# Kernel optimization log

Measured on AMD Instinct MI355X. Metric: run time of the kernel, lower is better.

## Reference

```python
import jax, jax.numpy as jnp
import numpy as np

B, H, W = 256, 512, 512
KH, KW = 16, 16
OH, OW = 8, 8
N = (H // KH) * (W // KW)  # 1024 chunks
KIN = KH * KW              # 256
KOUT = OH * OW             # 64


def setup_inputs() -> dict:
    key = jax.random.key(0)
    kx, kw, kb = jax.random.split(key, 3)
    x = jax.random.normal(kx, (B, H, W), dtype=jnp.float32)
    # Per-chunk Linear weights, torch-style uniform(-1/sqrt(fan_in), 1/sqrt(fan_in))
    bound = 1.0 / np.sqrt(KIN)
    Wk = jax.random.uniform(kw, (N, KOUT, KIN), dtype=jnp.float32, minval=-bound, maxval=bound)
    bk = jax.random.uniform(kb, (N, KOUT), dtype=jnp.float32, minval=-bound, maxval=bound)
    return {"x": x, "Wk": Wk, "bk": bk}


def _split_chunks(x):
    # [B,H,W] -> [B, N, KH, KW] matching split_matrix_in_chunks
    b = x.shape[0]
    return (x.reshape(b, H // KH, KH, W // KW, KW)
             .swapaxes(2, 3)
             .reshape(b, N, KH, KW))


def _recombine(chunks):
    # [B, N, OH, OW] -> [B, s*OH, s*OW] matching recombine_chunks_into_matrix
    b = chunks.shape[0]
    s = int(np.sqrt(N))
    return (chunks.reshape(b, s, s, OH, OW)
                  .swapaxes(3, 2)
                  .reshape(b, s * OH, s * OW))


def reference(x, Wk, bk):
    xc = _split_chunks(x).reshape(-1, N, KIN)          # [B,N,KIN]
    # grouped GEMM: one Linear per chunk, fused with bias + ReLU
    y = jnp.einsum('bnk,nok->bno', xc, Wk) + bk[None]  # [B,N,KOUT]
    y = jax.nn.relu(y)
    out = _recombine(y.reshape(-1, N, OH, OW))         # [B, s*OH, s*OW]
    b, h, w = out.shape
    return out.reshape(b, h * w)
```

## Files before the change

### kernel.cpp

```cpp
#include <hip/hip_runtime.h>


typedef __bf16 bf16x8 __attribute__((ext_vector_type(8)));
typedef float  f32x4  __attribute__((ext_vector_type(4)));

constexpr int LDW = 264;

union bfpack { unsigned short s[8]; bf16x8 v; };

__device__ __forceinline__ unsigned short f2bf(float f) {
  union { float f; unsigned u; } v; v.f = f;
  unsigned r = v.u + 0x7fffu + ((v.u >> 16) & 1u);
  return (unsigned short)(r >> 16);
}

typedef __attribute__((address_space(1))) const void GV;
typedef __attribute__((address_space(3))) void LV;

__global__ __launch_bounds__(256, 2) void comp_kernel(
    const float* __restrict__ x, const float* __restrict__ Wk,
    const float* __restrict__ bk, float* __restrict__ out) {
  __shared__ unsigned short Ws[64 * LDW];
  __shared__ float bs[64];
  __shared__ __align__(16) float Xs[4][2][1024];

  const int bid = blockIdx.x;
  const int n  = ((bid & 7) << 7) | (bid >> 3);
  const int ci = n >> 5, cj = n & 31;
  const int t = threadIdx.x;
  const int wave = t >> 6, lane = t & 63;
  const int m15 = lane & 15, quad = lane >> 4;

  const char* xbase = (const char*)x + (size_t)ci * 32768 + (size_t)cj * 64;
  const int b_hi = lane >> 4;
  const int rr = (lane & 15) * 16;

  auto stage_issue = [&](int s) {
    const int bp = s >> 2, q = s & 3;
    const int btile = bp * 64 + wave * 16;
    float* dst = &Xs[wave][s & 1][0];
    #pragma unroll
    for (int i = 0; i < 4; ++i) {
      const int b_it = i * 4 + b_hi;
      const int ro = rr ^ ((b_it & 7) << 4);
      const char* src = xbase + (size_t)(btile + b_it) * 1048576
                      + (size_t)((q * 4 + (ro >> 6)) * 2048 + (ro & 63));
      __builtin_amdgcn_global_load_lds((GV*)src, (LV*)(dst + i * 256), 16, 0, 0);
    }
  };

  stage_issue(0);
  stage_issue(1);

  const float4* wsrc = (const float4*)(Wk + (size_t)n * (64 * 256));
  #pragma unroll
  for (int it = 0; it < 8; ++it) {
    int i2 = it * 512 + t * 2;
    float4 g0 = wsrc[i2];
    float4 g1 = wsrc[i2 + 1];
    int o = i2 >> 6, pos = (i2 & 63) * 4;
    bfpack p;
    p.s[0] = f2bf(g0.x); p.s[1] = f2bf(g0.y); p.s[2] = f2bf(g0.z); p.s[3] = f2bf(g0.w);
    p.s[4] = f2bf(g1.x); p.s[5] = f2bf(g1.y); p.s[6] = f2bf(g1.z); p.s[7] = f2bf(g1.w);
    *(bf16x8*)&Ws[o * LDW + pos] = p.v;
  }
  if (t < 64) bs[t] = bk[n * 64 + t];
  __syncthreads();

  #pragma unroll
  for (int bp = 0; bp < 4; ++bp) {
    const int btile = bp * 64 + wave * 16;
    f32x4 acc[4] = {{0,0,0,0},{0,0,0,0},{0,0,0,0},{0,0,0,0}};

    #pragma unroll
    for (int q = 0; q < 4; ++q) {
      const int s = bp * 4 + q;
      if (s == 15)              asm volatile("s_waitcnt vmcnt(0)" ::: "memory");
      else if (s >= 4 && q < 2) asm volatile("s_waitcnt vmcnt(8)" ::: "memory");
      else                      asm volatile("s_waitcnt vmcnt(4)" ::: "memory");
      __builtin_amdgcn_sched_barrier(0);

      const char* Xb = (const char*)&Xs[wave][s & 1][0];
      const int sw = (m15 & 7) << 4;
      #pragma unroll
      for (int ksl = 0; ksl < 2; ++ksl) {
        const int c = ksl * 128 + quad * 32;
        float4 v0 = *(const float4*)(Xb + m15 * 256 + ((c)      ^ sw));
        float4 v1 = *(const float4*)(Xb + m15 * 256 + ((c + 16) ^ sw));
        bfpack a;
        a.s[0] = f2bf(v0.x); a.s[1] = f2bf(v0.y); a.s[2] = f2bf(v0.z); a.s[3] = f2bf(v0.w);
        a.s[4] = f2bf(v1.x); a.s[5] = f2bf(v1.y); a.s[6] = f2bf(v1.z); a.s[7] = f2bf(v1.w);

        const int ka = (q * 2 + ksl) * 32 + quad * 8;
        bf16x8 bb[4];
        #pragma unroll
        for (int nt = 0; nt < 4; ++nt)
          bb[nt] = *(const bf16x8*)&Ws[(nt * 16 + m15) * LDW + ka];
        #pragma unroll
        for (int nt = 0; nt < 4; ++nt)
          acc[nt] = __builtin_amdgcn_mfma_f32_16x16x32_bf16(bb[nt], a.v, acc[nt], 0, 0, 0);
      }

      if (s + 2 < 16) {
        __builtin_amdgcn_sched_barrier(0);
        stage_issue(s + 2);
        __builtin_amdgcn_sched_barrier(0);
      }
    }

    float* op = out + (size_t)(btile + m15) * 65536
                    + (size_t)(ci * 8) * 256 + cj * 8;
    #pragma unroll
    for (int nt = 0; nt < 4; ++nt) {
      const int o0 = nt * 16 + quad * 4;
      float4 b4 = *(const float4*)&bs[o0];
      float4 res;
      res.x = fmaxf(acc[nt][0] + b4.x, 0.f);
      res.y = fmaxf(acc[nt][1] + b4.y, 0.f);
      res.z = fmaxf(acc[nt][2] + b4.z, 0.f);
      res.w = fmaxf(acc[nt][3] + b4.w, 0.f);
      *(float4*)&op[(o0 >> 3) * 256 + (o0 & 7)] = res;
    }
  }
}

extern "C" void kernel_launch(void* const* d_in, const int* in_sizes, int n_in,
                              void* d_out, int out_size, void* d_ws, size_t ws_size,
                              hipStream_t stream) {
  const float* x  = (const float*)d_in[0];
  const float* Wk = (const float*)d_in[1];
  const float* bk = (const float*)d_in[2];
  float* out = (float*)d_out;
  comp_kernel<<<dim3(1024), dim3(256), 0, stream>>>(x, Wk, bk, out);
}
```

Before: 443.2 us.

## Pre-convert weights to MFMA-ready bf16 layout and process chunk pairs per block

Adds a separate pre-pass kernel that converts the fp32 per-chunk weights to bf16 in a fragment-ordered layout in workspace. The main kernel then loads weight fragments directly from global memory instead of staging them through LDS. Each block now covers two adjacent chunks with 512 threads, so every x load is a 128-byte row segment and gets a new swizzle. This removes the per-block LDS weight staging and the barrier, and widens x loads, at the cost of an extra kernel launch and a round trip of the weights through global memory.

```diff
diff --git a/kernel.cpp b/kernel.cpp
--- a/kernel.cpp
+++ b/kernel.cpp
@@ -3,8 +3,6 @@
 
 typedef __bf16 bf16x8 __attribute__((ext_vector_type(8)));
 typedef float  f32x4  __attribute__((ext_vector_type(4)));
-
-constexpr int LDW = 264;
 
 union bfpack { unsigned short s[8]; bf16x8 v; };
 
@@ -17,110 +15,125 @@
 typedef __attribute__((address_space(1))) const void GV;
 typedef __attribute__((address_space(3))) void LV;
 
-__global__ __launch_bounds__(256, 2) void comp_kernel(
-    const float* __restrict__ x, const float* __restrict__ Wk,
+__global__ __launch_bounds__(256) void wconv_kernel(
+    const float* __restrict__ Wk, unsigned short* __restrict__ Wc) {
+  const int n = blockIdx.x, t = threadIdx.x;
+  const float4* src = (const float4*)(Wk + (size_t)n * 16384);
+  unsigned short* dst = Wc + (size_t)n * 16384;
+  #pragma unroll
+  for (int it = 0; it < 16; ++it) {
+    const int idx = it * 256 + t;
+    float4 g = src[idx];
+    const int o = idx >> 6, kq = idx & 63;
+    const int ks = kq >> 3, quad = (kq >> 1) & 3, h = kq & 1;
+    ushort4 p;
+    p.x = f2bf(g.x); p.y = f2bf(g.y); p.z = f2bf(g.z); p.w = f2bf(g.w);
+    *(ushort4*)&dst[(size_t)((ks * 4 + (o >> 4)) * 64 + (quad * 16 + (o & 15))) * 8 + h * 4] = p;
+  }
+}
+
+__global__ __launch_bounds__(512, 4) void comp_kernel(
+    const float* __restrict__ x, const unsigned short* __restrict__ Wc,
     const float* __restrict__ bk, float* __restrict__ out) {
-  __shared__ unsigned short Ws[64 * LDW];
-  __shared__ float bs[64];
-  __shared__ __align__(16) float Xs[4][2][1024];
+  __shared__ float bs[128];
+  __shared__ __align__(16) char Xs[8][2][4096];
 
   const int bid = blockIdx.x;
-  const int n  = ((bid & 7) << 7) | (bid >> 3);
-  const int ci = n >> 5, cj = n & 31;
+  const int w = ((bid & 7) << 6) | (bid >> 3);
+  const int ci = w >> 4, cjp = w & 15;
   const int t = threadIdx.x;
   const int wave = t >> 6, lane = t & 63;
   const int m15 = lane & 15, quad = lane >> 4;
 
-  const char* xbase = (const char*)x + (size_t)ci * 32768 + (size_t)cj * 64;
-  const int b_hi = lane >> 4;
-  const int rr = (lane & 15) * 16;
+  const int n0 = ci * 32 + cjp * 2;
+
+  if (t < 32) *(float4*)&bs[t * 4] = *(const float4*)&bk[(size_t)n0 * 64 + t * 4];
+  __syncthreads();
+
+  const char* xb = (const char*)x + (size_t)ci * 32768 + (size_t)cjp * 128;
+  const int sgm = lane >> 3, g = lane & 7;
+  const int b_sub = sgm >> 1, r_dma = sgm & 1;
+
+  const int slab = ((m15 >> 2) << 10) | ((m15 & 3) << 8) | ((quad >> 1) << 7);
+  const int sw = m15 & 3;
+  const int c2_0 = (quad & 1) ^ sw;
+  const int c2_1 = (2 | (quad & 1)) ^ sw;
+
+  const unsigned short* wp0 = Wc + (size_t)n0 * 16384 + lane * 8;
 
   auto stage_issue = [&](int s) {
-    const int bp = s >> 2, q = s & 3;
-    const int btile = bp * 64 + wave * 16;
-    float* dst = &Xs[wave][s & 1][0];
+    const int grp = s >> 3, ks = s & 7;
+    char* dstb = &Xs[wave][s & 1][0];
     #pragma unroll
     for (int i = 0; i < 4; ++i) {
-      const int b_it = i * 4 + b_hi;
-      const int ro = rr ^ ((b_it & 7) << 4);
-      const char* src = xbase + (size_t)(btile + b_it) * 1048576
-                      + (size_t)((q * 4 + (ro >> 6)) * 2048 + (ro & 63));
-      __builtin_amdgcn_global_load_lds((GV*)src, (LV*)(dst + i * 256), 16, 0, 0);
+      const int bl = i * 4 + b_sub;
+      const int b  = wave * 32 + grp * 16 + bl;
+      const int col = (((g >> 1) ^ (bl & 3)) << 5) | ((g & 1) << 4);
+      const char* src = xb + (size_t)b * 1048576 + (2 * ks + r_dma) * 2048 + col;
+      __builtin_amdgcn_global_load_lds((GV*)src, (LV*)(dstb + i * 1024), 16, 0, 0);
     }
   };
 
   stage_issue(0);
   stage_issue(1);
 
-  const float4* wsrc = (const float4*)(Wk + (size_t)n * (64 * 256));
   #pragma unroll
-  for (int it = 0; it < 8; ++it) {
-    int i2 = it * 512 + t * 2;
-    float4 g0 = wsrc[i2];
-    float4 g1 = wsrc[i2 + 1];
-    int o = i2 >> 6, pos = (i2 & 63) * 4;
-    bfpack p;
-    p.s[0] = f2bf(g0.x); p.s[1] = f2bf(g0.y); p.s[2] = f2bf(g0.z); p.s[3] = f2bf(g0.w);
-    p.s[4] = f2bf(g1.x); p.s[5] = f2bf(g1.y); p.s[6] = f2bf(g1.z); p.s[7] = f2bf(g1.w);
-    *(bf16x8*)&Ws[o * LDW + pos] = p.v;
-  }
-  if (t < 64) bs[t] = bk[n * 64 + t];
-  __syncthreads();
-
-  #pragma unroll
-  for (int bp = 0; bp < 4; ++bp) {
-    const int btile = bp * 64 + wave * 16;
-    f32x4 acc[4] = {{0,0,0,0},{0,0,0,0},{0,0,0,0},{0,0,0,0}};
-
+  for (int grp = 0; grp < 2; ++grp) {
+    f32x4 acc[2][4] = {{{0,0,0,0},{0,0,0,0},{0,0,0,0},{0,0,0,0}},
+                       {{0,0,0,0},{0,0,0,0},{0,0,0,0},{0,0,0,0}}};
     #pragma unroll
-    for (int q = 0; q < 4; ++q) {
-      const int s = bp * 4 + q;
-      if (s == 15)              asm volatile("s_waitcnt vmcnt(0)" ::: "memory");
-      else if (s >= 4 && q < 2) asm volatile("s_waitcnt vmcnt(8)" ::: "memory");
-      else                      asm volatile("s_waitcnt vmcnt(4)" ::: "memory");
+    for (int ks = 0; ks < 8; ++ks) {
+      const int s = grp * 8 + ks;
+      if (s == 8) asm volatile("s_waitcnt vmcnt(12)" ::: "memory");
+      else        asm volatile("s_waitcnt vmcnt(4)"  ::: "memory");
       __builtin_amdgcn_sched_barrier(0);
 
-      const char* Xb = (const char*)&Xs[wave][s & 1][0];
-      const int sw = (m15 & 7) << 4;
+      bf16x8 bw[2][4];
       #pragma unroll
-      for (int ksl = 0; ksl < 2; ++ksl) {
-        const int c = ksl * 128 + quad * 32;
-        float4 v0 = *(const float4*)(Xb + m15 * 256 + ((c)      ^ sw));
-        float4 v1 = *(const float4*)(Xb + m15 * 256 + ((c + 16) ^ sw));
-        bfpack a;
-        a.s[0] = f2bf(v0.x); a.s[1] = f2bf(v0.y); a.s[2] = f2bf(v0.z); a.s[3] = f2bf(v0.w);
-        a.s[4] = f2bf(v1.x); a.s[5] = f2bf(v1.y); a.s[6] = f2bf(v1.z); a.s[7] = f2bf(v1.w);
-
-        const int ka = (q * 2 + ksl) * 32 + quad * 8;
-        bf16x8 bb[4];
+      for (int ch = 0; ch < 2; ++ch)
         #pragma unroll
         for (int nt = 0; nt < 4; ++nt)
-          bb[nt] = *(const bf16x8*)&Ws[(nt * 16 + m15) * LDW + ka];
-        #pragma unroll
-        for (int nt = 0; nt < 4; ++nt)
-          acc[nt] = __builtin_amdgcn_mfma_f32_16x16x32_bf16(bb[nt], a.v, acc[nt], 0, 0, 0);
-      }
+          bw[ch][nt] = *(const bf16x8*)(wp0 + (size_t)ch * 16384 + ks * 2048 + nt * 512);
+
+      const char* Xb = &Xs[wave][s & 1][0];
+      float4 u0 = *(const float4*)(Xb + slab + c2_0 * 32);
+      float4 u1 = *(const float4*)(Xb + slab + c2_0 * 32 + 16);
+      float4 u2 = *(const float4*)(Xb + slab + c2_1 * 32);
+      float4 u3 = *(const float4*)(Xb + slab + c2_1 * 32 + 16);
+      bfpack a0, a1;
+      a0.s[0] = f2bf(u0.x); a0.s[1] = f2bf(u0.y); a0.s[2] = f2bf(u0.z); a0.s[3] = f2bf(u0.w);
+      a0.s[4] = f2bf(u1.x); a0.s[5] = f2bf(u1.y); a0.s[6] = f2bf(u1.z); a0.s[7] = f2bf(u1.w);
+      a1.s[0] = f2bf(u2.x); a1.s[1] = f2bf(u2.y); a1.s[2] = f2bf(u2.z); a1.s[3] = f2bf(u2.w);
+      a1.s[4] = f2bf(u3.x); a1.s[5] = f2bf(u3.y); a1.s[6] = f2bf(u3.z); a1.s[7] = f2bf(u3.w);
 
       if (s + 2 < 16) {
         __builtin_amdgcn_sched_barrier(0);
         stage_issue(s + 2);
         __builtin_amdgcn_sched_barrier(0);
       }
+
+      #pragma unroll
+      for (int nt = 0; nt < 4; ++nt) {
+        acc[0][nt] = __builtin_amdgcn_mfma_f32_16x16x32_bf16(bw[0][nt], a0.v, acc[0][nt], 0, 0, 0);
+        acc[1][nt] = __builtin_amdgcn_mfma_f32_16x16x32_bf16(bw[1][nt], a1.v, acc[1][nt], 0, 0, 0);
+      }
     }
 
-    float* op = out + (size_t)(btile + m15) * 65536
-                    + (size_t)(ci * 8) * 256 + cj * 8;
+    const int b = wave * 32 + grp * 16 + m15;
+    float* op = out + (size_t)b * 65536 + (size_t)(ci * 8) * 256 + cjp * 16;
     #pragma unroll
-    for (int nt = 0; nt < 4; ++nt) {
-      const int o0 = nt * 16 + quad * 4;
-      float4 b4 = *(const float4*)&bs[o0];
-      float4 res;
-      res.x = fmaxf(acc[nt][0] + b4.x, 0.f);
-      res.y = fmaxf(acc[nt][1] + b4.y, 0.f);
-      res.z = fmaxf(acc[nt][2] + b4.z, 0.f);
-      res.w = fmaxf(acc[nt][3] + b4.w, 0.f);
-      *(float4*)&op[(o0 >> 3) * 256 + (o0 & 7)] = res;
-    }
+    for (int ch = 0; ch < 2; ++ch)
+      #pragma unroll
+      for (int nt = 0; nt < 4; ++nt) {
+        const int o0 = nt * 16 + quad * 4;
+        float4 b4 = *(const float4*)&bs[ch * 64 + o0];
+        float4 res;
+        res.x = fmaxf(acc[ch][nt][0] + b4.x, 0.f);
+        res.y = fmaxf(acc[ch][nt][1] + b4.y, 0.f);
+        res.z = fmaxf(acc[ch][nt][2] + b4.z, 0.f);
+        res.w = fmaxf(acc[ch][nt][3] + b4.w, 0.f);
+        *(float4*)&op[(o0 >> 3) * 256 + ch * 8 + (o0 & 7)] = res;
+      }
   }
 }
 
@@ -131,5 +144,7 @@
   const float* Wk = (const float*)d_in[1];
   const float* bk = (const float*)d_in[2];
   float* out = (float*)d_out;
-  comp_kernel<<<dim3(1024), dim3(256), 0, stream>>>(x, Wk, bk, out);
+  unsigned short* Wc = (unsigned short*)d_ws;
+  wconv_kernel<<<dim3(1024), dim3(256), 0, stream>>>(Wk, Wc);
+  comp_kernel<<<dim3(512), dim3(512), 0, stream>>>(x, Wc, bk, out);
 }
```

New measurement: 487.1 us. 9.9% more time.
